# Optimization experiments

Measured on AMD Instinct MI355X. Metric: run time of the kernel, lower is better.

The kernel has to match this reference:

```python
import jax, jax.numpy as jnp
import numpy as np

D_MODEL, D_STATE, EXPAND = 1024, 16, 2
D_INNER = EXPAND * D_MODEL
BATCH, SEQ = 4, 4096


def setup_inputs() -> dict:
    key = jax.random.key(0)
    ks = jax.random.split(key, 9)
    s = 0.02
    return {
        "x": jax.random.normal(ks[0], (BATCH, SEQ, D_MODEL), jnp.float32),
        # torch Linear weight [out,in] stored transposed here as [in,out]
        "W_in": jax.random.normal(ks[1], (D_MODEL, 2 * D_INNER), jnp.float32) * s,
        "conv_w": jax.random.normal(ks[2], (D_INNER, 1, 3), jnp.float32) * s,  # depthwise, groups=D_INNER
        "conv_b": jax.random.normal(ks[3], (D_INNER,), jnp.float32) * s,
        "W_B": jax.random.normal(ks[4], (D_INNER, D_STATE), jnp.float32) * s,
        "W_C": jax.random.normal(ks[5], (D_INNER, D_STATE), jnp.float32) * s,
        "A": jax.random.normal(ks[6], (D_STATE,), jnp.float32),
        "D": jnp.ones((D_INNER,), jnp.float32),
        "W_out": jax.random.normal(ks[7], (D_INNER, D_MODEL), jnp.float32) * s,
    }


def reference(x, W_in, conv_w, conv_b, W_B, W_C, A, D, W_out):
    d_inner = conv_w.shape[0]
    # input projection and split into main / residual gate paths
    xr = jnp.einsum("bld,de->ble", x, W_in)  # [B, L, 2*d_inner]
    x_main, res = xr[..., :d_inner], xr[..., d_inner:]
    # depthwise conv1d along seq (kernel 3, pad 1)
    xc = jax.lax.conv_general_dilated(
        x_main.transpose(0, 2, 1), conv_w, (1,), [(1, 1)],
        dimension_numbers=("NCH", "OIH", "NCH"), feature_group_count=d_inner)
    xc = (xc + conv_b[None, :, None]).transpose(0, 2, 1)  # [B, L, d_inner]
    xc = jax.nn.silu(xc)
    # selective-scan inputs
    Bt = jnp.einsum("bli,is->bls", xc, W_B)  # [B, L, d_state]
    Ct = jnp.einsum("bli,is->bls", xc, W_C)
    decay = jnp.exp(-jax.nn.softplus(A))  # exp(A_diag), [d_state]

    def step(state, bc):
        b_t, c_t = bc
        state = state * decay + b_t  # i=0: zeros*decay + B[0] == B[0]
        return state, jnp.sum(state * c_t, axis=-1)  # scalar per batch

    _, ys = jax.lax.scan(step, jnp.zeros_like(Bt[:, 0]),
                         (Bt.transpose(1, 0, 2), Ct.transpose(1, 0, 2)))
    ys = ys.T  # [B, L]
    y = ys[..., None] + xc * D  # broadcast scan output across d_inner
    y = y * jax.nn.silu(res)
    return jnp.einsum("bli,id->bld", y, W_out)
```

## Files before the change

### kernel.cpp

```cpp
#include <hip/hip_runtime.h>


typedef _Float16 half8 __attribute__((ext_vector_type(8)));
typedef float floatx4 __attribute__((ext_vector_type(4)));

#define D_MODEL 1024
#define D_INNER 2048
#define SEQ     4096
#define NBATCH  4
#define NROWS   (NBATCH * SEQ)
#define CHUNK   16
#define NCHUNK  (SEQ / CHUNK)
#define NTASK   (NBATCH * NCHUNK)

__device__ __forceinline__ void async16(_Float16* lds, const _Float16* g) {
    __builtin_amdgcn_global_load_lds((const __attribute__((address_space(1))) void*)g,
                                     (__attribute__((address_space(3))) void*)lds, 16, 0, 0);
}

__device__ __forceinline__ float siluf(float x) {
    return x / (1.f + __expf(-x));
}

__device__ __forceinline__ float decay_of(const float* A, int s) {
    return __expf(-log1pf(__expf(A[s])));
}


__global__ __launch_bounds__(256) void convert_f32_f16(const float* __restrict__ src,
                                                       _Float16* __restrict__ dst) {
    size_t idx = ((size_t)blockIdx.x * 256 + threadIdx.x) * 8;
    float4 a = *(const float4*)(src + idx);
    float4 b = *(const float4*)(src + idx + 4);
    half8 o = {(_Float16)a.x, (_Float16)a.y, (_Float16)a.z, (_Float16)a.w,
               (_Float16)b.x, (_Float16)b.y, (_Float16)b.z, (_Float16)b.w};
    *(half8*)(dst + idx) = o;
}

__global__ __launch_bounds__(256) void transpose_to_f16(const float* __restrict__ src,
                                                        _Float16* __restrict__ dst,
                                                        int K, int N) {
    __shared__ float tile[32][33];
    int n0 = blockIdx.x * 32, k0 = blockIdx.y * 32;
    int x = threadIdx.x, y = threadIdx.y;
#pragma unroll
    for (int r = 0; r < 32; r += 8)
        tile[y + r][x] = src[(size_t)(k0 + y + r) * N + (n0 + x)];
    __syncthreads();
#pragma unroll
    for (int r = 0; r < 32; r += 8)
        dst[(size_t)(n0 + y + r) * K + (k0 + x)] = (_Float16)tile[x][y + r];
}

__global__ __launch_bounds__(256) void convert_wbct(const float* __restrict__ WB,
                                                    const float* __restrict__ WC,
                                                    _Float16* __restrict__ WBCT) {
    int idx = blockIdx.x * 256 + threadIdx.x;
    int n = idx >> 11, k = idx & 2047;
    float v = (n < 16) ? WB[k * 16 + n] : WC[k * 16 + (n - 16)];
    WBCT[idx] = (_Float16)v;
}

template <typename OutT>
__global__ __launch_bounds__(256) void gemm_tn(const _Float16* __restrict__ A,
                                               const _Float16* __restrict__ BT,
                                               OutT* __restrict__ C,
                                               int M, int N, int K) {
    __shared__ __align__(16) _Float16 As[128 * 64];
    __shared__ __align__(16) _Float16 Bs[128 * 64];
    const int tid = threadIdx.x;
    const int wid = tid >> 6, lane = tid & 63;
    const int row0 = blockIdx.y * 128, col0 = blockIdx.x * 128;
    const int wm = (wid & 1) * 64, wn = (wid >> 1) * 64;

    floatx4 acc[4][4] = {};

    const int sr = lane >> 3;
    const int sc = ((lane & 7) ^ sr) * 8;
    const size_t aBase = (size_t)(row0 + wid * 32 + sr) * K + sc;
    const size_t bBase = (size_t)(col0 + wid * 32 + sr) * K + sc;
    _Float16* ldsA = As + wid * 2048;
    _Float16* ldsB = Bs + wid * 2048;

    const int fr = lane & 15, q = lane >> 4;
    const int frq = fr & 7;

    for (int k0 = 0; k0 < K; k0 += 64) {
        __syncthreads();
#pragma unroll
        for (int t = 0; t < 4; t++) {
            async16(ldsA + t * 512, A + aBase + (size_t)(t * 8) * K + k0);
            async16(ldsB + t * 512, BT + bBase + (size_t)(t * 8) * K + k0);
        }
        __syncthreads();
#pragma unroll
        for (int kk = 0; kk < 2; kk++) {
            const int sw = (((kk << 2) + q) ^ frq) * 8;
            half8 af[4], bf[4];
#pragma unroll
            for (int i = 0; i < 4; i++) {
                af[i] = *(const half8*)(As + (wm + i * 16 + fr) * 64 + sw);
                bf[i] = *(const half8*)(Bs + (wn + i * 16 + fr) * 64 + sw);
            }
#pragma unroll
            for (int i = 0; i < 4; i++)
#pragma unroll
                for (int j = 0; j < 4; j++)
                    acc[i][j] = __builtin_amdgcn_mfma_f32_16x16x32_f16(af[i], bf[j], acc[i][j], 0, 0, 0);
        }
    }

    const int er = (lane >> 4) * 4, ec = lane & 15;
#pragma unroll
    for (int i = 0; i < 4; i++)
#pragma unroll
        for (int j = 0; j < 4; j++)
#pragma unroll
            for (int r = 0; r < 4; r++) {
                int row = row0 + wm + i * 16 + er + r;
                int col = col0 + wn + j * 16 + ec;
                C[(size_t)row * N + col] = (OutT)acc[i][j][r];
            }
}

__global__ __launch_bounds__(256) void bc_gemm(const _Float16* __restrict__ A,
                                               const _Float16* __restrict__ BT,
                                               float* __restrict__ C) {
    const int K = D_INNER;
    __shared__ __align__(16) _Float16 As[64 * 64];
    __shared__ __align__(16) _Float16 Bs[32 * 64];
    const int tid = threadIdx.x, wid = tid >> 6, lane = tid & 63;
    const int row0 = blockIdx.x * 64;
    floatx4 acc[2] = {};

    const int srow = lane >> 3;
    const int scol = (lane & 7) * 8;
    const size_t aOff0 = (size_t)(row0 + wid * 16 + srow) * K + scol;
    const size_t aOff1 = aOff0 + (size_t)8 * K;
    const size_t bOff  = (size_t)(wid * 8 + srow) * K + scol;
    _Float16* ldsA = As + wid * 1024;
    _Float16* ldsB = Bs + wid * 512;
    const int fr = lane & 15, fc = (lane >> 4) * 8;

    for (int k0 = 0; k0 < K; k0 += 64) {
        __syncthreads();
        async16(ldsA,       A + aOff0 + k0);
        async16(ldsA + 512, A + aOff1 + k0);
        async16(ldsB,       BT + bOff + k0);
        __syncthreads();
#pragma unroll
        for (int s = 0; s < 2; s++) {
            half8 af = *(const half8*)(As + (wid * 16 + fr) * 64 + s * 32 + fc);
#pragma unroll
            for (int nj = 0; nj < 2; nj++) {
                half8 bf = *(const half8*)(Bs + (nj * 16 + fr) * 64 + s * 32 + fc);
                acc[nj] = __builtin_amdgcn_mfma_f32_16x16x32_f16(af, bf, acc[nj], 0, 0, 0);
            }
        }
    }
    const int er = (lane >> 4) * 4, ec = lane & 15;
#pragma unroll
    for (int nj = 0; nj < 2; nj++)
#pragma unroll
        for (int r = 0; r < 4; r++)
            C[(size_t)(row0 + wid * 16 + er + r) * 32 + nj * 16 + ec] = acc[nj][r];
}

__global__ __launch_bounds__(256) void conv_silu(const _Float16* __restrict__ xr,
                                                 const float* __restrict__ cw,
                                                 const float* __restrict__ cb,
                                                 _Float16* __restrict__ xc) {
    int row = blockIdx.x;
    int l = row & (SEQ - 1);
    int i = threadIdx.x * 8;
    const _Float16* cur = xr + (size_t)row * 4096 + i;
    half8 c8 = *(const half8*)cur;
    half8 p8 = {}, n8 = {};
    if (l > 0)       p8 = *(const half8*)(cur - 4096);
    if (l < SEQ - 1) n8 = *(const half8*)(cur + 4096);
    half8 o;
#pragma unroll
    for (int j = 0; j < 8; j++) {
        int ii = i + j;
        float a = (float)p8[j] * cw[ii * 3] + (float)c8[j] * cw[ii * 3 + 1] +
                  (float)n8[j] * cw[ii * 3 + 2] + cb[ii];
        o[j] = (_Float16)siluf(a);
    }
    *(half8*)(xc + (size_t)row * D_INNER + i) = o;
}


__global__ __launch_bounds__(256) void scan_p1(const float* __restrict__ BtCt,
                                               const float* __restrict__ A,
                                               float* __restrict__ fin) {
    int g = blockIdx.x * 256 + threadIdx.x;
    int task = g >> 4, s = g & 15;
    int b = task >> 8, c = task & (NCHUNK - 1);
    const float decay = decay_of(A, s);
    size_t r = ((size_t)b * SEQ + c * CHUNK) * 32;
    float st = 0.f;
#pragma unroll
    for (int j = 0; j < CHUNK; j++)
        st = st * decay + BtCt[r + (size_t)j * 32 + s];
    fin[task * 16 + s] = st;
}

__global__ __launch_bounds__(64) void scan_p2(const float* __restrict__ fin,
                                              const float* __restrict__ A,
                                              float* __restrict__ carry) {
    int t = threadIdx.x;
    int b = t >> 4, s = t & 15;
    float decay = decay_of(A, s);
    float d16 = decay;
#pragma unroll
    for (int k = 0; k < 4; k++) d16 *= d16;
    float cy = 0.f;
    for (int c = 0; c < NCHUNK; c++) {
        int idx = ((b * NCHUNK) + c) * 16 + s;
        carry[idx] = cy;
        cy = cy * d16 + fin[idx];
    }
}

__global__ __launch_bounds__(256) void scan_p3_fuse(const float* __restrict__ BtCt,
                                                    const float* __restrict__ A,
                                                    const float* __restrict__ carry,
                                                    const float* __restrict__ D,
                                                    const _Float16* __restrict__ xr,
                                                    _Float16* __restrict__ xc) {
    __shared__ float ysl[CHUNK];
    const int task = blockIdx.x;
    const int b = task >> 8, c = task & (NCHUNK - 1);
    const int row0 = b * SEQ + c * CHUNK;
    const int tid = threadIdx.x;

    if (tid < 16) {
        const int s = tid;
        const float decay = decay_of(A, s);
        float st = carry[task * 16 + s];
        size_t r = (size_t)row0 * 32;
#pragma unroll
        for (int j = 0; j < CHUNK; j++) {
            st = st * decay + BtCt[r + s];
            float y = st * BtCt[r + 16 + s];
            y += __shfl_xor(y, 1, 16);
            y += __shfl_xor(y, 2, 16);
            y += __shfl_xor(y, 4, 16);
            y += __shfl_xor(y, 8, 16);
            if (s == 0) ysl[j] = y;
            r += 32;
        }
    }
    __syncthreads();

#pragma unroll
    for (int it = 0; it < 16; it++) {
        int chunk = it * 256 + tid;
        int rl = chunk >> 8;
        int colb = (chunk & 255) * 8;
        size_t row = (size_t)(row0 + rl);
        float yv = ysl[rl];
        half8 x8 = *(const half8*)(xc + row * D_INNER + colb);
        half8 r8 = *(const half8*)(xr + row * 4096 + 2048 + colb);
        float4 d0 = *(const float4*)(D + colb);
        float4 d1 = *(const float4*)(D + colb + 4);
        half8 o;
        float dd[8] = {d0.x, d0.y, d0.z, d0.w, d1.x, d1.y, d1.z, d1.w};
#pragma unroll
        for (int j = 0; j < 8; j++) {
            float y = yv + (float)x8[j] * dd[j];
            o[j] = (_Float16)(y * siluf((float)r8[j]));
        }
        *(half8*)(xc + row * D_INNER + colb) = o;
    }
}

extern "C" void kernel_launch(void* const* d_in, const int* in_sizes, int n_in,
                              void* d_out, int out_size, void* d_ws, size_t ws_size,
                              hipStream_t stream) {
    const float* x      = (const float*)d_in[0];
    const float* W_in   = (const float*)d_in[1];
    const float* conv_w = (const float*)d_in[2];
    const float* conv_b = (const float*)d_in[3];
    const float* W_B    = (const float*)d_in[4];
    const float* W_C    = (const float*)d_in[5];
    const float* A      = (const float*)d_in[6];
    const float* D      = (const float*)d_in[7];
    const float* W_out  = (const float*)d_in[8];
    float* out = (float*)d_out;

    char* ws = (char*)d_ws;
    size_t off = 0;
    auto alloc = [&](size_t bytes) { size_t o = off; off += (bytes + 255) & ~(size_t)255; return o; };
    _Float16* xh    = (_Float16*)(ws + alloc((size_t)NROWS * D_MODEL * 2));
    _Float16* WinT  = (_Float16*)(ws + alloc((size_t)4096 * 1024 * 2));
    _Float16* WoutT = (_Float16*)(ws + alloc((size_t)1024 * 2048 * 2));
    _Float16* WBCT  = (_Float16*)(ws + alloc((size_t)32 * 2048 * 2));
    _Float16* xr    = (_Float16*)(ws + alloc((size_t)NROWS * 4096 * 2));
    _Float16* xc    = (_Float16*)(ws + alloc((size_t)NROWS * D_INNER * 2));
    float*    BtCt  = (float*)(ws + alloc((size_t)NROWS * 32 * 4));
    float*    fin   = (float*)(ws + alloc((size_t)NTASK * 16 * 4));
    float*    carry = (float*)(ws + alloc((size_t)NTASK * 16 * 4));

    convert_f32_f16<<<(NROWS * D_MODEL) / (256 * 8), 256, 0, stream>>>(x, xh);
    transpose_to_f16<<<dim3(4096 / 32, 1024 / 32), dim3(32, 8), 0, stream>>>(W_in, WinT, 1024, 4096);
    transpose_to_f16<<<dim3(1024 / 32, 2048 / 32), dim3(32, 8), 0, stream>>>(W_out, WoutT, 2048, 1024);
    convert_wbct<<<(32 * 2048) / 256, 256, 0, stream>>>(W_B, W_C, WBCT);
    gemm_tn<_Float16><<<dim3(4096 / 128, NROWS / 128), 256, 0, stream>>>(xh, WinT, xr, NROWS, 4096, 1024);
    conv_silu<<<NROWS, 256, 0, stream>>>(xr, conv_w, conv_b, xc);
    bc_gemm<<<NROWS / 64, 256, 0, stream>>>(xc, WBCT, BtCt);
    scan_p1<<<NTASK * 16 / 256, 256, 0, stream>>>(BtCt, A, fin);
    scan_p2<<<1, 64, 0, stream>>>(fin, A, carry);
    scan_p3_fuse<<<NTASK, 256, 0, stream>>>(BtCt, A, carry, D, xr, xc);
    gemm_tn<float><<<dim3(1024 / 128, NROWS / 128), 256, 0, stream>>>(xc, WoutT, out, NROWS, 1024, 2048);
}
```

Measured before the change: 518.3 us.

## Fuse conv+SiLU, B/C projection and scan pass 1 into one per-chunk kernel

Replaces three kernels (depthwise conv+SiLU, MFMA B/C projection GEMM, chunk-local scan) with a single kernel per 16-row chunk. Each block runs the conv over its chunk with a sliding window of rows, writes xc, re-reads it (likely from cache) to compute the B/C dot products with scalar FMAs and cross-lane/LDS reductions, then runs the chunk-final scan state. This removes two launches and the separate xc/BtCt round trips, but gives up MFMA for the B/C projection in favour of scalar math, with heavy per-thread register accumulators. It also unrolls the scan_p2 carry loop.

```diff
diff --git a/kernel.cpp b/kernel.cpp
--- a/kernel.cpp
+++ b/kernel.cpp
@@ -123,86 +123,108 @@
             }
 }
 
-__global__ __launch_bounds__(256) void bc_gemm(const _Float16* __restrict__ A,
-                                               const _Float16* __restrict__ BT,
-                                               float* __restrict__ C) {
-    const int K = D_INNER;
-    __shared__ __align__(16) _Float16 As[64 * 64];
-    __shared__ __align__(16) _Float16 Bs[32 * 64];
-    const int tid = threadIdx.x, wid = tid >> 6, lane = tid & 63;
-    const int row0 = blockIdx.x * 64;
-    floatx4 acc[2] = {};
-
-    const int srow = lane >> 3;
-    const int scol = (lane & 7) * 8;
-    const size_t aOff0 = (size_t)(row0 + wid * 16 + srow) * K + scol;
-    const size_t aOff1 = aOff0 + (size_t)8 * K;
-    const size_t bOff  = (size_t)(wid * 8 + srow) * K + scol;
-    _Float16* ldsA = As + wid * 1024;
-    _Float16* ldsB = Bs + wid * 512;
-    const int fr = lane & 15, fc = (lane >> 4) * 8;
-
-    for (int k0 = 0; k0 < K; k0 += 64) {
-        __syncthreads();
-        async16(ldsA,       A + aOff0 + k0);
-        async16(ldsA + 512, A + aOff1 + k0);
-        async16(ldsB,       BT + bOff + k0);
-        __syncthreads();
-#pragma unroll
-        for (int s = 0; s < 2; s++) {
-            half8 af = *(const half8*)(As + (wid * 16 + fr) * 64 + s * 32 + fc);
-#pragma unroll
-            for (int nj = 0; nj < 2; nj++) {
-                half8 bf = *(const half8*)(Bs + (nj * 16 + fr) * 64 + s * 32 + fc);
-                acc[nj] = __builtin_amdgcn_mfma_f32_16x16x32_f16(af, bf, acc[nj], 0, 0, 0);
-            }
-        }
-    }
-    const int er = (lane >> 4) * 4, ec = lane & 15;
-#pragma unroll
-    for (int nj = 0; nj < 2; nj++)
-#pragma unroll
-        for (int r = 0; r < 4; r++)
-            C[(size_t)(row0 + wid * 16 + er + r) * 32 + nj * 16 + ec] = acc[nj][r];
-}
-
-__global__ __launch_bounds__(256) void conv_silu(const _Float16* __restrict__ xr,
-                                                 const float* __restrict__ cw,
-                                                 const float* __restrict__ cb,
-                                                 _Float16* __restrict__ xc) {
-    int row = blockIdx.x;
-    int l = row & (SEQ - 1);
-    int i = threadIdx.x * 8;
-    const _Float16* cur = xr + (size_t)row * 4096 + i;
-    half8 c8 = *(const half8*)cur;
-    half8 p8 = {}, n8 = {};
-    if (l > 0)       p8 = *(const half8*)(cur - 4096);
-    if (l < SEQ - 1) n8 = *(const half8*)(cur + 4096);
-    half8 o;
-#pragma unroll
-    for (int j = 0; j < 8; j++) {
-        int ii = i + j;
-        float a = (float)p8[j] * cw[ii * 3] + (float)c8[j] * cw[ii * 3 + 1] +
-                  (float)n8[j] * cw[ii * 3 + 2] + cb[ii];
-        o[j] = (_Float16)siluf(a);
-    }
-    *(half8*)(xc + (size_t)row * D_INNER + i) = o;
-}
-
-
-__global__ __launch_bounds__(256) void scan_p1(const float* __restrict__ BtCt,
-                                               const float* __restrict__ A,
-                                               float* __restrict__ fin) {
-    int g = blockIdx.x * 256 + threadIdx.x;
-    int task = g >> 4, s = g & 15;
-    int b = task >> 8, c = task & (NCHUNK - 1);
-    const float decay = decay_of(A, s);
-    size_t r = ((size_t)b * SEQ + c * CHUNK) * 32;
-    float st = 0.f;
-#pragma unroll
-    for (int j = 0; j < CHUNK; j++)
-        st = st * decay + BtCt[r + (size_t)j * 32 + s];
-    fin[task * 16 + s] = st;
+__global__ __launch_bounds__(256) void conv_bc_p1(const _Float16* __restrict__ xr,
+                                                  const float* __restrict__ cw,
+                                                  const float* __restrict__ cb,
+                                                  const _Float16* __restrict__ WBCT,
+                                                  const float* __restrict__ A,
+                                                  _Float16* __restrict__ xc,
+                                                  float* __restrict__ BtCt,
+                                                  float* __restrict__ fin) {
+    const int task = blockIdx.x;
+    const int b = task >> 8, c = task & (NCHUNK - 1);
+    const int row0 = b * SEQ + c * CHUNK;
+    const int tid = threadIdx.x;
+
+    {
+        const int col0 = tid * 8;
+        float w0[8], w1[8], w2[8], bb[8];
+#pragma unroll
+        for (int j = 0; j < 8; j++) {
+            w0[j] = cw[(col0 + j) * 3];
+            w1[j] = cw[(col0 + j) * 3 + 1];
+            w2[j] = cw[(col0 + j) * 3 + 2];
+            bb[j] = cb[col0 + j];
+        }
+        half8 prev = {}, cur, next;
+        if (c > 0) prev = *(const half8*)(xr + (size_t)(row0 - 1) * 4096 + col0);
+        cur = *(const half8*)(xr + (size_t)row0 * 4096 + col0);
+#pragma unroll
+        for (int r = 0; r < CHUNK; r++) {
+            if (c == NCHUNK - 1 && r == CHUNK - 1) {
+                half8 z = {};
+                next = z;
+            } else {
+                next = *(const half8*)(xr + (size_t)(row0 + r + 1) * 4096 + col0);
+            }
+            half8 o;
+#pragma unroll
+            for (int j = 0; j < 8; j++) {
+                float a = (float)prev[j] * w0[j] + (float)cur[j] * w1[j] +
+                          (float)next[j] * w2[j] + bb[j];
+                o[j] = (_Float16)siluf(a);
+            }
+            *(half8*)(xc + (size_t)(row0 + r) * D_INNER + col0) = o;
+            prev = cur;
+            cur = next;
+        }
+    }
+    __syncthreads();
+
+    const int cg = tid >> 4, s = tid & 15;
+    float accB[CHUNK], accC[CHUNK];
+#pragma unroll
+    for (int r = 0; r < CHUNK; r++) { accB[r] = 0.f; accC[r] = 0.f; }
+
+    const int colb0 = cg * 128;
+#pragma unroll 4
+    for (int kc = 0; kc < 16; kc++) {
+        const int colb = colb0 + kc * 8;
+        half8 wb8 = *(const half8*)(WBCT + (size_t)s * D_INNER + colb);
+        half8 wc8 = *(const half8*)(WBCT + (size_t)(16 + s) * D_INNER + colb);
+#pragma unroll
+        for (int r = 0; r < CHUNK; r++) {
+            half8 x8 = *(const half8*)(xc + (size_t)(row0 + r) * D_INNER + colb);
+#pragma unroll
+            for (int j = 0; j < 8; j++) {
+                accB[r] += (float)x8[j] * (float)wb8[j];
+                accC[r] += (float)x8[j] * (float)wc8[j];
+            }
+        }
+    }
+
+    __shared__ float red[4 * CHUNK * 32];
+    __shared__ float btl[CHUNK * 32];
+    const int wid = tid >> 6, lane = tid & 63;
+#pragma unroll
+    for (int r = 0; r < CHUNK; r++) {
+        float vb = accB[r], vc = accC[r];
+        vb += __shfl_xor(vb, 16); vb += __shfl_xor(vb, 32);
+        vc += __shfl_xor(vc, 16); vc += __shfl_xor(vc, 32);
+        if ((lane >> 4) == 0) {
+            red[wid * (CHUNK * 32) + r * 32 + s] = vb;
+            red[wid * (CHUNK * 32) + r * 32 + 16 + s] = vc;
+        }
+    }
+    __syncthreads();
+#pragma unroll
+    for (int i = 0; i < 2; i++) {
+        int idx = tid * 2 + i;
+        int r = idx >> 5, o = idx & 31;
+        float v = red[r * 32 + o] + red[(CHUNK * 32) + r * 32 + o] +
+                  red[2 * (CHUNK * 32) + r * 32 + o] + red[3 * (CHUNK * 32) + r * 32 + o];
+        btl[idx] = v;
+        BtCt[(size_t)(row0 + r) * 32 + o] = v;
+    }
+    __syncthreads();
+    if (tid < 16) {
+        const float decay = decay_of(A, tid);
+        float st = 0.f;
+#pragma unroll
+        for (int r = 0; r < CHUNK; r++)
+            st = st * decay + btl[r * 32 + tid];
+        fin[task * 16 + tid] = st;
+    }
 }
 
 __global__ __launch_bounds__(64) void scan_p2(const float* __restrict__ fin,
@@ -215,6 +237,7 @@
 #pragma unroll
     for (int k = 0; k < 4; k++) d16 *= d16;
     float cy = 0.f;
+#pragma unroll 8
     for (int c = 0; c < NCHUNK; c++) {
         int idx = ((b * NCHUNK) + c) * 16 + s;
         carry[idx] = cy;
@@ -307,9 +330,7 @@
     transpose_to_f16<<<dim3(1024 / 32, 2048 / 32), dim3(32, 8), 0, stream>>>(W_out, WoutT, 2048, 1024);
     convert_wbct<<<(32 * 2048) / 256, 256, 0, stream>>>(W_B, W_C, WBCT);
     gemm_tn<_Float16><<<dim3(4096 / 128, NROWS / 128), 256, 0, stream>>>(xh, WinT, xr, NROWS, 4096, 1024);
-    conv_silu<<<NROWS, 256, 0, stream>>>(xr, conv_w, conv_b, xc);
-    bc_gemm<<<NROWS / 64, 256, 0, stream>>>(xc, WBCT, BtCt);
-    scan_p1<<<NTASK * 16 / 256, 256, 0, stream>>>(BtCt, A, fin);
+    conv_bc_p1<<<NTASK, 256, 0, stream>>>(xr, conv_w, conv_b, WBCT, A, xc, BtCt, fin);
     scan_p2<<<1, 64, 0, stream>>>(fin, A, carry);
     scan_p3_fuse<<<NTASK, 256, 0, stream>>>(BtCt, A, carry, D, xr, xc);
     gemm_tn<float><<<dim3(1024 / 128, NROWS / 128), 256, 0, stream>>>(xc, WoutT, out, NROWS, 1024, 2048);
```

Result: slower. 552.3 us (+6.6%).
